# Optimization experiments

Hardware: AMD Instinct MI355X
Metric: run time of the kernel (lower is better)

Reference implementation:

```python
import jax, jax.numpy as jnp
import numpy as np

BN_EPS = 1e-5
TN_EPS = 1e-4


def binarize(x):
    # Clipped straight-through binarization (Courbariaux BNN / Brevitas 1-bit):
    # forward = sign(x) in {-1,+1}, backward = hardtanh STE.
    xc = jnp.clip(x, -1.0, 1.0)
    return xc + jax.lax.stop_gradient(jnp.where(x >= 0, 1.0, -1.0).astype(x.dtype) - xc)


def setup_inputs() -> dict:
    key = jax.random.key(0)
    ks = jax.random.split(key, 20)
    B, D, H, C = 16384, 1024, 1024, 10
    inp = {"x": jax.random.uniform(ks[0], (B, D), dtype=jnp.float32)}
    dims = [(H, D), (H, H), (H, H), (C, H)]
    for i, (o, n) in enumerate(dims):
        inp[f"W{i+1}"] = jax.random.uniform(ks[1 + i], (o, n), minval=-1.0, maxval=1.0, dtype=jnp.float32)
    # BatchNorm1d params (eval mode, running stats) for the 3 hidden layers
    for i in range(3):
        k0, k1, k2, k3 = jax.random.split(ks[5 + i], 4)
        inp[f"g{i+1}"] = 1.0 + 0.1 * jax.random.normal(k0, (H,), dtype=jnp.float32)
        inp[f"b{i+1}"] = 0.1 * jax.random.normal(k1, (H,), dtype=jnp.float32)
        inp[f"m{i+1}"] = 0.1 * jax.random.normal(k2, (H,), dtype=jnp.float32)
        inp[f"v{i+1}"] = 0.5 + jax.random.uniform(k3, (H,), dtype=jnp.float32)
    # TensorNorm (scalar norm on the logits)
    inp["tn_w"] = jnp.ones((), dtype=jnp.float32)
    inp["tn_b"] = jnp.zeros((), dtype=jnp.float32)
    inp["tn_m"] = jnp.zeros((), dtype=jnp.float32)
    inp["tn_v"] = jnp.ones((), dtype=jnp.float32)
    return inp


def reference(x, W1, W2, W3, W4,
              g1, b1, m1, v1,
              g2, b2, m2, v2,
              g3, b3, m3, v3,
              tn_w, tn_b, tn_m, tn_v):
    h = binarize(2.0 * x.reshape(x.shape[0], -1) - 1.0)
    # Dropout is identity in eval mode.
    bn = [(g1, b1, m1, v1), (g2, b2, m2, v2), (g3, b3, m3, v3)]
    for W, (g, b, m, v) in zip((W1, W2, W3), bn):
        h = h @ binarize(W).T                      # [B,H] fake-quant linear, no bias
        h = (h - m) * (g * jax.lax.rsqrt(v + BN_EPS)) + b  # BatchNorm1d eval
        h = binarize(h)                            # 1-bit activation quant
    h = h @ binarize(W4).T                         # [B,10]
    # TensorNorm: scalar affine normalization over the whole tensor
    return (h - tn_m) * jax.lax.rsqrt(tn_v + TN_EPS) * tn_w + tn_b
```

## Files before the change

### kernel.cpp

```cpp
#include <hip/hip_runtime.h>
#include <stdint.h>

typedef int   v4i  __attribute__((ext_vector_type(4)));
typedef int   v8i  __attribute__((ext_vector_type(8)));
typedef float v16f __attribute__((ext_vector_type(16)));
typedef unsigned int uint32;

#define BATCH 16384
#define FEAT  1024

#define OFF_ACTA 0u
#define OFF_ACTB 16777216u
#define OFF_WA1  33554432u
#define OFF_WA2  34603008u
#define OFF_WA3  35651584u
#define OFF_WA4  36700160u
#define OFF_TH   36732928u

__device__ __forceinline__ uint32 nib8(uint32 lo, uint32 hb) {
    uint32 r = 0u;
#pragma unroll
    for (int j = 0; j < 4; ++j) {
        uint32 b = (lo >> (8 * j)) & 0xFFu;
        r |= (((b & 8u) | ((b & 1u) << 1)) << (4 * j));
    }
#pragma unroll
    for (int j = 0; j < 4; ++j) {
        uint32 b = (hb >> (8 * j)) & 0xFFu;
        r |= (((b & 8u) | ((b & 1u) << 1)) << (4 * j + 16));
    }
    return r;
}

__global__ void __launch_bounds__(256) prep_kernel(
    const float* __restrict__ x,
    const float* __restrict__ W1, const float* __restrict__ W2,
    const float* __restrict__ W3, const float* __restrict__ W4,
    const float* __restrict__ g1, const float* __restrict__ b1,
    const float* __restrict__ m1, const float* __restrict__ v1,
    const float* __restrict__ g2, const float* __restrict__ b2,
    const float* __restrict__ m2, const float* __restrict__ v2,
    const float* __restrict__ g3, const float* __restrict__ b3,
    const float* __restrict__ m3, const float* __restrict__ v3,
    char* __restrict__ actA, char* __restrict__ wa1, char* __restrict__ wa2,
    char* __restrict__ wa3, char* __restrict__ wa4, int* __restrict__ TH)
{
    int b = blockIdx.x;
    if (b == 609) {
        for (int gid = threadIdx.x; gid < 3072; gid += 256) {
            int l = gid >> 10, j = gid & 1023;
            const float *g, *bb, *m, *v;
            if (l == 0)      { g = g1; bb = b1; m = m1; v = v1; }
            else if (l == 1) { g = g2; bb = b2; m = m2; v = v2; }
            else             { g = g3; bb = b3; m = m3; v = v3; }
            double gd = (double)g[j], bd = (double)bb[j], md = (double)m[j], vd = (double)v[j];
            double s = gd / sqrt(vd + 1e-5);
            int t2;
            if (s > 0.0)      t2 = (int)ceil(md - bd / s);
            else if (s < 0.0) t2 = -(int)floor(md - bd / s);
            else              t2 = (bd >= 0.0) ? -2000000 : 2000000;
            int sidx = (j >> 5) * 32 + ((j >> 2) & 1) * 16 + (j & 3) + 4 * ((j & 31) >> 3);
            TH[l * 1024 + sidx] = t2;
        }
        return;
    }

    const float* src; char* dst; float thr; int nrows; int dblk;
    const float* gp = nullptr;
    if (b < 512)      { src = x  + (size_t)b * 32768;            dst = actA; dblk = b;      thr = 0.5f; nrows = 32; }
    else if (b < 544) { int mb = b - 512; src = W1 + (size_t)mb * 32768; dst = wa1; dblk = mb; thr = 0.0f; nrows = 32; gp = g1; }
    else if (b < 576) { int mb = b - 544; src = W2 + (size_t)mb * 32768; dst = wa2; dblk = mb; thr = 0.0f; nrows = 32; gp = g2; }
    else if (b < 608) { int mb = b - 576; src = W3 + (size_t)mb * 32768; dst = wa3; dblk = mb; thr = 0.0f; nrows = 32; gp = g3; }
    else              { src = W4; dst = wa4; dblk = 0; thr = 0.0f; nrows = 10; }

    __shared__ unsigned char T[32][1040];
#pragma unroll
    for (int u = 0; u < 8; ++u) {
        int unit = threadIdx.x + u * 256;
        int row  = unit >> 6;
        int c16  = (unit & 63) << 4;
        uint32 wb0 = 0, wb1 = 0, wb2 = 0, wb3 = 0;
        if (row < nrows) {
            bool flipb = gp && (gp[dblk * 32 + row] < 0.0f);
            const float* p = src + (size_t)row * 1024 + c16;
            float4 f0 = *(const float4*)(p + 0);
            float4 f1 = *(const float4*)(p + 4);
            float4 f2 = *(const float4*)(p + 8);
            float4 f3 = *(const float4*)(p + 12);
#define BY(f) ((((f) >= thr) != flipb) ? 0x01u : 0xFFu)
            wb0 = BY(f0.x) | (BY(f0.y)<<8) | (BY(f0.z)<<16) | (BY(f0.w)<<24);
            wb1 = BY(f1.x) | (BY(f1.y)<<8) | (BY(f1.z)<<16) | (BY(f1.w)<<24);
            wb2 = BY(f2.x) | (BY(f2.y)<<8) | (BY(f2.z)<<16) | (BY(f2.w)<<24);
            wb3 = BY(f3.x) | (BY(f3.y)<<8) | (BY(f3.z)<<16) | (BY(f3.w)<<24);
#undef BY
        }
        *(uint4*)&T[row][c16] = make_uint4(wb0, wb1, wb2, wb3);
    }
    __syncthreads();

    int lane = threadIdx.x & 63;
    int wq   = threadIdx.x >> 6;
    int c    = lane & 31;
    int hi   = lane >> 5;
#pragma unroll
    for (int u = 0; u < 4; ++u) {
        int f = wq * 4 + u;
        uint32 dw0, dw1, dw2, dw3;
        {
            int base = 64 * f + 4 * hi;
            dw0 = nib8(*(const uint32*)&T[c][base],      *(const uint32*)&T[c][base + 8]);
            dw1 = nib8(*(const uint32*)&T[c][base + 16], *(const uint32*)&T[c][base + 24]);
            dw2 = nib8(*(const uint32*)&T[c][base + 32], *(const uint32*)&T[c][base + 40]);
            dw3 = nib8(*(const uint32*)&T[c][base + 48], *(const uint32*)&T[c][base + 56]);
        }
        *(uint4*)(dst + (((size_t)dblk * 16 + f) * 64 + lane) * 16) = make_uint4(dw0, dw1, dw2, dw3);
    }
}

__device__ __forceinline__ void gload16(const v4i* gsrc, v4i* ldst) {
    __builtin_amdgcn_global_load_lds(
        (const __attribute__((address_space(1))) void*)gsrc,
        (__attribute__((address_space(3))) void*)ldst, 16, 0, 0);
}

__device__ __forceinline__ v16f MFMA4(v4i a, v4i b, v16f c) {
    v8i av; av[0] = a[0]; av[1] = a[1]; av[2] = a[2]; av[3] = a[3];
    av[4] = 0; av[5] = 0; av[6] = 0; av[7] = 0;
    v8i bv; bv[0] = b[0]; bv[1] = b[1]; bv[2] = b[2]; bv[3] = b[3];
    bv[4] = 0; bv[5] = 0; bv[6] = 0; bv[7] = 0;
    return __builtin_amdgcn_mfma_scale_f32_32x32x64_f8f6f4(
        av, bv, c, 4, 4, 0, 0x7F7F7F7F, 0, 0x7F7F7F7F);
}

__global__ void __launch_bounds__(1024, 4) net_kernel(
    const v4i* __restrict__ Xp,  const v4i* __restrict__ Wp1,
    const v4i* __restrict__ Wp2, const v4i* __restrict__ Wp3,
    const v4i* __restrict__ Wp4, const int* __restrict__ TH,
    const float* __restrict__ tw, const float* __restrict__ tb,
    const float* __restrict__ tm, const float* __restrict__ tv,
    float* __restrict__ out)
{
    __shared__ v4i Hs[2048];
    __shared__ v4i Wb[2][2048];
    const int tid  = threadIdx.x;
    const int lane = tid & 63;
    const int wv   = tid >> 6;
    const int hi   = lane >> 5;
    const int blk  = blockIdx.x;

    {
        const v4i* src = Xp + (size_t)blk * 2048;
#pragma unroll
        for (int j = 0; j < 2; ++j)
            gload16(src + j * 1024 + wv * 64 + lane, &Hs[j * 1024 + wv * 64]);
        gload16(Wp1 + (size_t)(wv * 16) * 64 + lane,        &Wb[0][wv * 64]);
        gload16(Wp1 + (size_t)((16 + wv) * 16) * 64 + lane, &Wb[0][1024 + wv * 64]);
    }
    asm volatile("s_waitcnt vmcnt(0)" ::: "memory");
    __syncthreads();

    const int mt0 = wv * 2, mt1 = wv * 2 + 1;

#pragma unroll 1
    for (int l = 0; l < 3; ++l) {
        const v4i* W = (l == 0) ? Wp1 : (l == 1) ? Wp2 : Wp3;
        const int* thl = TH + l * 1024;

        v16f acc00, acc01, acc10, acc11;
        {
            const int4* t0 = (const int4*)(thl + mt0 * 32 + hi * 16);
            const int4* t1 = (const int4*)(thl + mt1 * 32 + hi * 16);
#pragma unroll
            for (int g = 0; g < 4; ++g) {
                int4 ta = t0[g], tc = t1[g];
                acc00[4*g+0] = -(float)ta.x; acc00[4*g+1] = -(float)ta.y;
                acc00[4*g+2] = -(float)ta.z; acc00[4*g+3] = -(float)ta.w;
                acc10[4*g+0] = -(float)tc.x; acc10[4*g+1] = -(float)tc.y;
                acc10[4*g+2] = -(float)tc.z; acc10[4*g+3] = -(float)tc.w;
            }
#pragma unroll
            for (int q = 0; q < 16; ++q) { acc01[q] = acc00[q]; acc11[q] = acc10[q]; }
        }

#pragma unroll 1
        for (int fs = 0; fs < 16; ++fs) {
            const int cur = fs & 1;
            const v4i* Wc = &Wb[cur][0];
            v4i* Wn = &Wb[cur ^ 1][0];
            if (fs < 15) {
                gload16(W + (size_t)(wv * 16 + fs + 1) * 64 + lane,        Wn + wv * 64);
                gload16(W + (size_t)((16 + wv) * 16 + fs + 1) * 64 + lane, Wn + 1024 + wv * 64);
            } else if (l < 2) {
                const v4i* W2 = (l == 0) ? Wp2 : Wp3;
                gload16(W2 + (size_t)(wv * 16) * 64 + lane,        Wn + wv * 64);
                gload16(W2 + (size_t)((16 + wv) * 16) * 64 + lane, Wn + 1024 + wv * 64);
            }
            v4i a0 = Wc[mt0 * 64 + lane];
            v4i a1 = Wc[mt1 * 64 + lane];
            v4i b0 = Hs[fs * 64 + lane];
            v4i b1 = Hs[(16 + fs) * 64 + lane];
            acc00 = MFMA4(a0, b0, acc00);
            acc01 = MFMA4(a0, b1, acc01);
            acc10 = MFMA4(a1, b0, acc10);
            acc11 = MFMA4(a1, b1, acc11);
            asm volatile("s_waitcnt vmcnt(0)" ::: "memory");
            __builtin_amdgcn_s_barrier();
        }

#define NB4(h) (((h) >= 0.0f) ? 2u : 10u)
        uint32 p00a = 0, p00b = 0, p01a = 0, p01b = 0;
        uint32 p10a = 0, p10b = 0, p11a = 0, p11b = 0;
#pragma unroll
        for (int j = 0; j < 8; ++j) {
            p00a |= NB4(acc00[j]) << (4 * j);  p00b |= NB4(acc00[8 + j]) << (4 * j);
            p01a |= NB4(acc01[j]) << (4 * j);  p01b |= NB4(acc01[8 + j]) << (4 * j);
            p10a |= NB4(acc10[j]) << (4 * j);  p10b |= NB4(acc10[8 + j]) << (4 * j);
            p11a |= NB4(acc11[j]) << (4 * j);  p11b |= NB4(acc11[8 + j]) << (4 * j);
        }
#undef NB4

        __syncthreads();
        {
            v4i o;
            o[0] = (int)p00a; o[1] = (int)p00b; o[2] = (int)p10a; o[3] = (int)p10b;
            Hs[(0 * 16 + wv) * 64 + lane] = o;
            o[0] = (int)p01a; o[1] = (int)p01b; o[2] = (int)p11a; o[3] = (int)p11b;
            Hs[(16 + wv) * 64 + lane] = o;
        }
        __syncthreads();
    }

    if (wv < 2) {
        const int nb = wv;
        v16f acc;
#pragma unroll
        for (int z = 0; z < 16; ++z) acc[z] = 0.0f;
#pragma unroll
        for (int f = 0; f < 16; ++f) {
            v4i av = Wp4[f * 64 + lane];
            v4i bv = Hs[(nb * 16 + f) * 64 + lane];
            acc = MFMA4(av, bv, acc);
        }
        double sc  = (double)tw[0] / sqrt((double)tv[0] + 1e-4);
        double off = (double)tb[0] - (double)tm[0] * sc;
        int colg = blk * 64 + nb * 32 + (lane & 31);
#pragma unroll
        for (int q = 0; q < 8; ++q) {
            int rr = (q & 3) + 8 * (q >> 2) + 4 * hi;
            if (rr < 10)
                out[(size_t)colg * 10 + rr] = (float)((double)acc[q] * sc + off);
        }
    }
}

extern "C" void kernel_launch(void* const* d_in, const int* in_sizes, int n_in,
                              void* d_out, int out_size, void* d_ws, size_t ws_size,
                              hipStream_t stream) {
    const float* x  = (const float*)d_in[0];
    const float* W1 = (const float*)d_in[1];
    const float* W2 = (const float*)d_in[2];
    const float* W3 = (const float*)d_in[3];
    const float* W4 = (const float*)d_in[4];
    const float* g1 = (const float*)d_in[5];
    const float* b1 = (const float*)d_in[6];
    const float* m1 = (const float*)d_in[7];
    const float* v1 = (const float*)d_in[8];
    const float* g2 = (const float*)d_in[9];
    const float* b2 = (const float*)d_in[10];
    const float* m2 = (const float*)d_in[11];
    const float* v2 = (const float*)d_in[12];
    const float* g3 = (const float*)d_in[13];
    const float* b3 = (const float*)d_in[14];
    const float* m3 = (const float*)d_in[15];
    const float* v3 = (const float*)d_in[16];
    const float* tw = (const float*)d_in[17];
    const float* tb = (const float*)d_in[18];
    const float* tm = (const float*)d_in[19];
    const float* tv = (const float*)d_in[20];

    char* ws = (char*)d_ws;
    char* actA = ws + OFF_ACTA;
    char* wa1  = ws + OFF_WA1;
    char* wa2  = ws + OFF_WA2;
    char* wa3  = ws + OFF_WA3;
    char* wa4  = ws + OFF_WA4;
    int*  TH   = (int*)(ws + OFF_TH);

    prep_kernel<<<610, 256, 0, stream>>>(x, W1, W2, W3, W4,
                                         g1, b1, m1, v1, g2, b2, m2, v2,
                                         g3, b3, m3, v3,
                                         actA, wa1, wa2, wa3, wa4, TH);

    net_kernel<<<256, 1024, 0, stream>>>((const v4i*)actA,
                                         (const v4i*)wa1, (const v4i*)wa2,
                                         (const v4i*)wa3, (const v4i*)wa4,
                                         TH, tw, tb, tm, tv, (float*)d_out);
}
```

Baseline: 189.6 us.

## Deepen weight prefetch pipeline from double to triple buffering

Adds a third LDS weight buffer so weight tiles are prefetched two steps ahead. Waits use vmcnt(2) instead of draining all loads, so one stage of global loads stays in flight across each barrier. The intent is to hide global load latency behind the MFMA work. The cost is 32KB more LDS per block, which may limit occupancy. The wait accounting is subtle, and any vmcnt mismatch, for example around the activation stores at layer end, could cause races.

```diff
diff --git a/kernel.cpp b/kernel.cpp
--- a/kernel.cpp
+++ b/kernel.cpp
@@ -141,7 +141,7 @@
     float* __restrict__ out)
 {
     __shared__ v4i Hs[2048];
-    __shared__ v4i Wb[2][2048];
+    __shared__ v4i Wb[3][2048];
     const int tid  = threadIdx.x;
     const int lane = tid & 63;
     const int wv   = tid >> 6;
@@ -150,20 +150,21 @@
 
     {
         const v4i* src = Xp + (size_t)blk * 2048;
-#pragma unroll
-        for (int j = 0; j < 2; ++j)
-            gload16(src + j * 1024 + wv * 64 + lane, &Hs[j * 1024 + wv * 64]);
-        gload16(Wp1 + (size_t)(wv * 16) * 64 + lane,        &Wb[0][wv * 64]);
-        gload16(Wp1 + (size_t)((16 + wv) * 16) * 64 + lane, &Wb[0][1024 + wv * 64]);
-    }
-    asm volatile("s_waitcnt vmcnt(0)" ::: "memory");
-    __syncthreads();
+        gload16(src + 0 * 1024 + wv * 64 + lane, &Hs[0 * 1024 + wv * 64]);
+        gload16(src + 1 * 1024 + wv * 64 + lane, &Hs[1 * 1024 + wv * 64]);
+        gload16(Wp1 + (size_t)(wv * 16 + 0) * 64 + lane,        &Wb[0][wv * 64]);
+        gload16(Wp1 + (size_t)((16 + wv) * 16 + 0) * 64 + lane, &Wb[0][1024 + wv * 64]);
+        gload16(Wp1 + (size_t)(wv * 16 + 1) * 64 + lane,        &Wb[1][wv * 64]);
+        gload16(Wp1 + (size_t)((16 + wv) * 16 + 1) * 64 + lane, &Wb[1][1024 + wv * 64]);
+    }
+    asm volatile("s_waitcnt vmcnt(2)" ::: "memory");
+    __builtin_amdgcn_s_barrier();
 
     const int mt0 = wv * 2, mt1 = wv * 2 + 1;
+    int bcur = 0;
 
 #pragma unroll 1
     for (int l = 0; l < 3; ++l) {
-        const v4i* W = (l == 0) ? Wp1 : (l == 1) ? Wp2 : Wp3;
         const int* thl = TH + l * 1024;
 
         v16f acc00, acc01, acc10, acc11;
@@ -184,17 +185,20 @@
 
 #pragma unroll 1
         for (int fs = 0; fs < 16; ++fs) {
-            const int cur = fs & 1;
-            const v4i* Wc = &Wb[cur][0];
-            v4i* Wn = &Wb[cur ^ 1][0];
-            if (fs < 15) {
-                gload16(W + (size_t)(wv * 16 + fs + 1) * 64 + lane,        Wn + wv * 64);
-                gload16(W + (size_t)((16 + wv) * 16 + fs + 1) * 64 + lane, Wn + 1024 + wv * 64);
+            const v4i* Wc = &Wb[bcur][0];
+            const int bstg = (bcur + 2 >= 3) ? (bcur - 1) : (bcur + 2);
+            v4i* Wn = &Wb[bstg][0];
+            bool tail = false;
+            if (fs < 14) {
+                const v4i* W = (l == 0) ? Wp1 : (l == 1) ? Wp2 : Wp3;
+                gload16(W + (size_t)(wv * 16 + fs + 2) * 64 + lane,        Wn + wv * 64);
+                gload16(W + (size_t)((16 + wv) * 16 + fs + 2) * 64 + lane, Wn + 1024 + wv * 64);
             } else if (l < 2) {
                 const v4i* W2 = (l == 0) ? Wp2 : Wp3;
-                gload16(W2 + (size_t)(wv * 16) * 64 + lane,        Wn + wv * 64);
-                gload16(W2 + (size_t)((16 + wv) * 16) * 64 + lane, Wn + 1024 + wv * 64);
-            }
+                gload16(W2 + (size_t)(wv * 16 + fs - 14) * 64 + lane,        Wn + wv * 64);
+                gload16(W2 + (size_t)((16 + wv) * 16 + fs - 14) * 64 + lane, Wn + 1024 + wv * 64);
+            } else tail = true;
+
             v4i a0 = Wc[mt0 * 64 + lane];
             v4i a1 = Wc[mt1 * 64 + lane];
             v4i b0 = Hs[fs * 64 + lane];
@@ -203,8 +207,11 @@
             acc01 = MFMA4(a0, b1, acc01);
             acc10 = MFMA4(a1, b0, acc10);
             acc11 = MFMA4(a1, b1, acc11);
-            asm volatile("s_waitcnt vmcnt(0)" ::: "memory");
+
+            if (tail) asm volatile("s_waitcnt vmcnt(0)" ::: "memory");
+            else      asm volatile("s_waitcnt vmcnt(2)" ::: "memory");
             __builtin_amdgcn_s_barrier();
+            bcur = (bcur == 2) ? 0 : bcur + 1;
         }
 
 #define NB4(h) (((h) >= 0.0f) ? 2u : 10u)
```

Result: faster. 183.4 us (-3.2%).
